# Kernel tuning notes

Measured on AMD Instinct MI355X. Metric: run time of the kernel, lower is better.

Reference implementation:

```python
import jax, jax.numpy as jnp
import numpy as np

N = 100000      # nodes
E = 1600000     # directed edges
F_IN = 128      # num_node_features
C = 10          # num_classes
EPS = 1e-5      # BatchNorm eps


def setup_inputs() -> dict:
    key = jax.random.key(0)
    ks = jax.random.split(key, 16)
    x = jax.random.normal(ks[0], (N, F_IN), jnp.float32)
    edge_index = jax.random.randint(ks[1], (2, E), 0, N, dtype=jnp.int32)

    def glorot(k, fi, fo):
        s = jnp.sqrt(6.0 / (fi + fo)).astype(jnp.float32)
        return jax.random.uniform(k, (fi, fo), jnp.float32, -s, s)

    return {
        "x": x, "edge_index": edge_index,
        "W1": glorot(ks[2], F_IN, 16), "b1": jnp.zeros((16,), jnp.float32),
        "g1": jnp.ones((16,), jnp.float32), "be1": jnp.zeros((16,), jnp.float32),
        "W2": glorot(ks[3], 16, 32), "b2": jnp.zeros((32,), jnp.float32),
        "g2": jnp.ones((32,), jnp.float32), "be2": jnp.zeros((32,), jnp.float32),
        "W3": glorot(ks[4], 32, 64), "b3": jnp.zeros((64,), jnp.float32),
        "g3": jnp.ones((64,), jnp.float32), "be3": jnp.zeros((64,), jnp.float32),
        "W4": glorot(ks[5], 64, C), "b4": jnp.zeros((C,), jnp.float32),
    }


def _gcn_conv(h, W, b, src, dst, norm):
    # GCNConv: transform then normalized scatter-add aggregation (with self-loops baked into src/dst/norm)
    h = h @ W                                   # [N, F_out]
    msg = h[src] * norm[:, None]                # [E+N, F_out] edge-gathered messages
    agg = jax.ops.segment_sum(msg, dst, num_segments=N)
    return agg + b


def _bn_gelu(h, g, be):
    # BatchNorm1d (training-mode batch stats, biased var) + exact GELU
    mu = h.mean(axis=0)
    var = ((h - mu) ** 2).mean(axis=0)
    return jax.nn.gelu((h - mu) * jax.lax.rsqrt(var + EPS) * g + be, approximate=False)


def reference(x, edge_index, W1, b1, g1, be1, W2, b2, g2, be2, W3, b3, g3, be3, W4, b4):
    src, dst = edge_index[0], edge_index[1]
    loop = jnp.arange(N, dtype=src.dtype)
    src = jnp.concatenate([src, loop])          # add self-loops
    dst = jnp.concatenate([dst, loop])
    deg = jax.ops.segment_sum(jnp.ones_like(dst, jnp.float32), dst, num_segments=N)
    dinv = jax.lax.rsqrt(deg)                   # deg >= 1 thanks to self-loops
    norm = dinv[src] * dinv[dst]                # D^-1/2 (A+I) D^-1/2 edge weights

    h = _bn_gelu(_gcn_conv(x, W1, b1, src, dst, norm), g1, be1)
    h = _bn_gelu(_gcn_conv(h, W2, b2, src, dst, norm), g2, be2)
    h = _bn_gelu(_gcn_conv(h, W3, b3, src, dst, norm), g3, be3)
    # dropout is identity in eval mode
    h = _gcn_conv(h, W4, b4, src, dst, norm)
    return jax.nn.log_softmax(h, axis=1)
```

## Files before the change

kernel.cpp:

```cpp
#include <hip/hip_runtime.h>
#include <math.h>


#define TPB 256
#define K_BUCK 256
#define CCHUNK 4096
#define DCAP 8192
constexpr float BN_EPS = 1e-5f;

#define SCHUNK 2048

__global__ void scan_reduce_kernel(const int* __restrict__ in, int* __restrict__ bsum, int n) {
    int base = blockIdx.x * SCHUNK;
    int s = 0;
    for (int j = threadIdx.x; j < SCHUNK; j += TPB) {
        int i = base + j;
        s += (i < n) ? in[i] : 0;
    }
#pragma unroll
    for (int d = 32; d; d >>= 1) s += __shfl_down(s, d);
    __shared__ int ws[TPB / 64];
    if ((threadIdx.x & 63) == 0) ws[threadIdx.x >> 6] = s;
    __syncthreads();
    if (threadIdx.x == 0) {
        int t = 0;
        for (int w = 0; w < TPB / 64; ++w) t += ws[w];
        bsum[blockIdx.x] = t;
    }
}

__global__ void scan_bsum_kernel(int* __restrict__ bsum, int nb) {
    __shared__ int carry;
    int lane = threadIdx.x;
    if (lane == 0) carry = 0;
    __syncthreads();
    for (int base = 0; base < nb; base += 64) {
        int i = base + lane;
        int v = (i < nb) ? bsum[i] : 0;
        int incl = v;
#pragma unroll
        for (int d = 1; d < 64; d <<= 1) {
            int u = __shfl_up(incl, d);
            if (lane >= d) incl += u;
        }
        if (i < nb) bsum[i] = carry + incl - v;
        int tot = __shfl(incl, 63);
        __syncthreads();
        if (lane == 0) carry += tot;
        __syncthreads();
    }
}

__global__ void scan_apply_kernel(const int* __restrict__ in, const int* __restrict__ bsum,
                                  int* __restrict__ out, int n) {
    int base = blockIdx.x * SCHUNK;
    int tid = threadIdx.x;
    int lane = tid & 63, wave = tid >> 6;
    int i0 = base + tid * 8;
    int v[8];
    int tsum = 0;
#pragma unroll
    for (int k = 0; k < 8; ++k) {
        int i = i0 + k;
        v[k] = (i < n) ? in[i] : 0;
        tsum += v[k];
    }
    int incl = tsum;
#pragma unroll
    for (int d = 1; d < 64; d <<= 1) {
        int u = __shfl_up(incl, d);
        if (lane >= d) incl += u;
    }
    int lexcl = incl - tsum;
    __shared__ int wsum[TPB / 64];
    if (lane == 63) wsum[wave] = incl;
    __syncthreads();
    int wbase = 0;
    for (int w = 0; w < wave; ++w) wbase += wsum[w];
    int off = bsum[blockIdx.x] + wbase + lexcl;
#pragma unroll
    for (int k = 0; k < 8; ++k) {
        int i = i0 + k;
        if (i < n) out[i] = off;
        off += v[k];
    }
}


__global__ void bucket_hist_kernel(const int* __restrict__ dst, int* __restrict__ hist,
                                   float* __restrict__ stats, int e, int n, int nb) {
    __shared__ int lh[K_BUCK];
    for (int i = threadIdx.x; i < K_BUCK; i += TPB) lh[i] = 0;
    if (blockIdx.x == 0)
        for (int i = threadIdx.x; i < 384; i += TPB) stats[i] = 0.0f;
    __syncthreads();
    int base = blockIdx.x * CCHUNK;
    int end = min(base + CCHUNK, e);
    int div = (n + K_BUCK - 1) / K_BUCK;
    for (int i = base + threadIdx.x; i < end; i += TPB) atomicAdd(&lh[dst[i] / div], 1);
    __syncthreads();
    for (int b = threadIdx.x; b < K_BUCK; b += TPB) hist[b * nb + blockIdx.x] = lh[b];
}

__global__ void bucket_scatter_kernel(const int* __restrict__ src, const int* __restrict__ dst,
                                      const int* __restrict__ hist, const int* __restrict__ hbase,
                                      int2* __restrict__ ebuf, int e, int n, int nb) {
    __shared__ int lbase[K_BUCK];
    __shared__ int eoff[K_BUCK];
    __shared__ int lcur[K_BUCK];
    __shared__ int2 stage[CCHUNK];
    int t = threadIdx.x;
    int blk = blockIdx.x;
    int c = hist[t * nb + blk];
    lbase[t] = hbase[t * nb + blk];
    lcur[t] = 0;
    eoff[t] = c;
    __syncthreads();
    for (int d = 1; d < K_BUCK; d <<= 1) {
        int v = (t >= d) ? eoff[t - d] : 0;
        __syncthreads();
        eoff[t] += v;
        __syncthreads();
    }
    eoff[t] -= c;
    __syncthreads();
    int base = blk * CCHUNK;
    int end = min(base + CCHUNK, e);
    int div = (n + K_BUCK - 1) / K_BUCK;
    for (int i = base + t; i < end; i += TPB) {
        int d = dst[i];
        int b = d / div;
        int p = atomicAdd(&lcur[b], 1);
        stage[eoff[b] + p] = make_int2(src[i], d);
    }
    __syncthreads();
    int cnt_here = end - base;
    for (int j = t; j < cnt_here; j += TPB) {
        int2 e2 = stage[j];
        int b = e2.y / div;
        ebuf[lbase[b] + (j - eoff[b])] = e2;
    }
}

__global__ void bucket_offsets_kernel(const int2* __restrict__ ebuf, const int* __restrict__ hbase,
                                      int* __restrict__ offsets, float* __restrict__ dinv,
                                      int e, int n, int nb) {
    __shared__ int lcnt[512];
    __shared__ int lexc[512];
    int b = blockIdx.x;
    int div = (n + K_BUCK - 1) / K_BUCK;
    int lo = b * div;
    int hi = min(lo + div, n);
    int nloc = hi - lo;
    int ebeg = hbase[b * nb];
    int eend = (b == K_BUCK - 1) ? e : hbase[(b + 1) * nb];
    for (int i = threadIdx.x; i < 512; i += TPB) lcnt[i] = 0;
    __syncthreads();
    for (int j = ebeg + threadIdx.x; j < eend; j += TPB)
        atomicAdd(&lcnt[ebuf[j].y - lo], 1);
    __syncthreads();
    if (threadIdx.x < 64) {
        int l = threadIdx.x;
        int base = l * 8;
        int v[8];
        int tsum = 0;
#pragma unroll
        for (int k = 0; k < 8; ++k) { v[k] = lcnt[base + k]; tsum += v[k]; }
        int incl = tsum;
#pragma unroll
        for (int d = 1; d < 64; d <<= 1) {
            int u = __shfl_up(incl, d);
            if (l >= d) incl += u;
        }
        int off = incl - tsum;
#pragma unroll
        for (int k = 0; k < 8; ++k) { lexc[base + k] = off; off += v[k]; }
    }
    __syncthreads();
    for (int i = threadIdx.x; i < nloc; i += TPB) {
        offsets[lo + i] = ebeg + lexc[i];
        dinv[lo + i] = rsqrtf((float)(lcnt[i] + 1));
    }
    if (b == K_BUCK - 1 && threadIdx.x == 0) offsets[n] = e;
}

__global__ void csr_fill_kernel(const int2* __restrict__ ebuf, const int* __restrict__ hbase,
                                const int* __restrict__ offsets, int* __restrict__ csr_src,
                                int e, int n, int nb) {
    __shared__ int lcur[400];
    __shared__ int lcsr[DCAP];
    int b = blockIdx.x;
    int div = (n + K_BUCK - 1) / K_BUCK;
    int lo = b * div;
    int hi = min(lo + div, n);
    int ebeg = hbase[b * nb];
    int eend = (b == K_BUCK - 1) ? e : hbase[(b + 1) * nb];
    int segbase = offsets[lo];
    int seglen = eend - ebeg;
    for (int i = threadIdx.x; i < hi - lo; i += TPB) lcur[i] = offsets[lo + i] - segbase;
    __syncthreads();
    for (int j = ebeg + threadIdx.x; j < eend; j += TPB) {
        int2 e2 = ebuf[j];
        int p = atomicAdd(&lcur[e2.y - lo], 1);
        if (p < DCAP) lcsr[p] = e2.x;
        else csr_src[segbase + p] = e2.x;
    }
    __syncthreads();
    int lim = min(seglen, DCAP);
    for (int j = threadIdx.x; j < lim; j += TPB) csr_src[segbase + j] = lcsr[j];
}


template <int FIN, int FOUT, bool DINV>
__global__ void gemm_rw_kernel(const float* __restrict__ H, const float* __restrict__ W,
                               float* __restrict__ O, const float* __restrict__ dinv, int n) {
    int row = blockIdx.x * blockDim.x + threadIdx.x;
    if (row >= n) return;
    float acc[FOUT];
#pragma unroll
    for (int c = 0; c < FOUT; ++c) acc[c] = 0.0f;
    const float4* h4 = (const float4*)(H + (size_t)row * FIN);
#pragma unroll
    for (int k = 0; k < FIN / 4; ++k) {
        float4 h = h4[k];
        const float* w = W + (size_t)(4 * k) * FOUT;
#pragma unroll
        for (int c = 0; c < FOUT; ++c) {
            acc[c] = fmaf(h.x, w[c], acc[c]);
            acc[c] = fmaf(h.y, w[FOUT + c], acc[c]);
            acc[c] = fmaf(h.z, w[2 * FOUT + c], acc[c]);
            acc[c] = fmaf(h.w, w[3 * FOUT + c], acc[c]);
        }
    }
    float sc = DINV ? dinv[row] : 1.0f;
    float4* o4 = (float4*)(O + (size_t)row * FOUT);
#pragma unroll
    for (int c = 0; c < FOUT / 4; ++c)
        o4[c] = make_float4(acc[4 * c] * sc, acc[4 * c + 1] * sc,
                            acc[4 * c + 2] * sc, acc[4 * c + 3] * sc);
}

__global__ void gemm_l4_kernel(const float* __restrict__ H, const float* __restrict__ W,
                               float* __restrict__ O, const float* __restrict__ dinv, int n) {
    int row = blockIdx.x * blockDim.x + threadIdx.x;
    if (row >= n) return;
    float acc[10];
#pragma unroll
    for (int c = 0; c < 10; ++c) acc[c] = 0.0f;
    const float4* h4 = (const float4*)(H + (size_t)row * 64);
#pragma unroll
    for (int k = 0; k < 16; ++k) {
        float4 h = h4[k];
        const float* w = W + (size_t)(4 * k) * 10;
#pragma unroll
        for (int c = 0; c < 10; ++c) {
            acc[c] = fmaf(h.x, w[c], acc[c]);
            acc[c] = fmaf(h.y, w[10 + c], acc[c]);
            acc[c] = fmaf(h.z, w[20 + c], acc[c]);
            acc[c] = fmaf(h.w, w[30 + c], acc[c]);
        }
    }
    float sc = dinv[row];
    float4* o4 = (float4*)(O + (size_t)row * 16);
    o4[0] = make_float4(acc[0] * sc, acc[1] * sc, acc[2] * sc, acc[3] * sc);
    o4[1] = make_float4(acc[4] * sc, acc[5] * sc, acc[6] * sc, acc[7] * sc);
    o4[2] = make_float4(acc[8] * sc, acc[9] * sc, 0.0f, 0.0f);
}

template <int F>
__global__ void bn_stats_kernel(const float* __restrict__ V, float* __restrict__ stats, int n) {
    constexpr int RPB = TPB / F;
    int f = threadIdx.x % F;
    int rl = threadIdx.x / F;
    float s = 0.0f, s2 = 0.0f;
    for (int r = blockIdx.x * RPB + rl; r < n; r += gridDim.x * RPB) {
        float v = V[(size_t)r * F + f];
        s += v;
        s2 = fmaf(v, v, s2);
    }
    __shared__ float sh[2 * F];
    for (int i = threadIdx.x; i < 2 * F; i += TPB) sh[i] = 0.0f;
    __syncthreads();
    atomicAdd(&sh[f], s);
    atomicAdd(&sh[F + f], s2);
    __syncthreads();
    for (int i = threadIdx.x; i < 2 * F; i += TPB) atomicAdd(&stats[i], sh[i]);
}


template <int F, bool STATS>
__global__ void agg4_kernel(const float* __restrict__ T, float* __restrict__ A,
                            const float* __restrict__ dinv, const int* __restrict__ offsets,
                            const int* __restrict__ csr_src, float* __restrict__ stats, int n) {
    constexpr int G = F / 4;
    __shared__ float sh[STATS ? 2 * F : 1];
    if (STATS) {
        for (int i = threadIdx.x; i < 2 * F; i += blockDim.x) sh[i] = 0.0f;
        __syncthreads();
    }
    const float4* T4 = (const float4*)T;
    float4 ss = {0, 0, 0, 0}, s2 = {0, 0, 0, 0};
    int lane0 = -1;
    int total = n * G;
    int stride = gridDim.x * blockDim.x;
    for (int idx = blockIdx.x * blockDim.x + threadIdx.x; idx < total; idx += stride) {
        int node = idx / G;
        int lane = idx % G;
        float4 acc = T4[(size_t)node * G + lane];
        int s = offsets[node], e = offsets[node + 1];
        int j = s;
        for (; j + 3 < e; j += 4) {
            int u0 = csr_src[j], u1 = csr_src[j + 1], u2 = csr_src[j + 2], u3 = csr_src[j + 3];
            float4 t0 = T4[(size_t)u0 * G + lane];
            float4 t1 = T4[(size_t)u1 * G + lane];
            float4 t2 = T4[(size_t)u2 * G + lane];
            float4 t3 = T4[(size_t)u3 * G + lane];
            acc.x += (t0.x + t1.x) + (t2.x + t3.x);
            acc.y += (t0.y + t1.y) + (t2.y + t3.y);
            acc.z += (t0.z + t1.z) + (t2.z + t3.z);
            acc.w += (t0.w + t1.w) + (t2.w + t3.w);
        }
        for (; j < e; ++j) {
            int u = csr_src[j];
            float4 t = T4[(size_t)u * G + lane];
            acc.x += t.x; acc.y += t.y; acc.z += t.z; acc.w += t.w;
        }
        float di = dinv[node];
        acc.x *= di; acc.y *= di; acc.z *= di; acc.w *= di;
        ((float4*)A)[(size_t)idx] = acc;
        if (STATS) {
            ss.x += acc.x; ss.y += acc.y; ss.z += acc.z; ss.w += acc.w;
            s2.x = fmaf(acc.x, acc.x, s2.x); s2.y = fmaf(acc.y, acc.y, s2.y);
            s2.z = fmaf(acc.z, acc.z, s2.z); s2.w = fmaf(acc.w, acc.w, s2.w);
            lane0 = lane;
        }
    }
    if (STATS) {
        if (lane0 >= 0) {
            atomicAdd(&sh[lane0 * 4 + 0], ss.x); atomicAdd(&sh[lane0 * 4 + 1], ss.y);
            atomicAdd(&sh[lane0 * 4 + 2], ss.z); atomicAdd(&sh[lane0 * 4 + 3], ss.w);
            atomicAdd(&sh[F + lane0 * 4 + 0], s2.x); atomicAdd(&sh[F + lane0 * 4 + 1], s2.y);
            atomicAdd(&sh[F + lane0 * 4 + 2], s2.z); atomicAdd(&sh[F + lane0 * 4 + 3], s2.w);
        }
        __syncthreads();
        for (int i = threadIdx.x; i < 2 * F; i += blockDim.x) atomicAdd(&stats[i], sh[i]);
    }
}

__global__ void agg_lsm_kernel(const float* __restrict__ T, const float* __restrict__ dinv,
                               const int* __restrict__ offsets, const int* __restrict__ csr_src,
                               const float* __restrict__ b4, float* __restrict__ out, int n) {
    int idx = blockIdx.x * blockDim.x + threadIdx.x;
    int node = idx >> 2;
    int lane = idx & 3;
    if (node >= n) return;
    const float4* T4 = (const float4*)T;
    float4 acc = T4[(size_t)node * 4 + lane];
    int s = offsets[node], e = offsets[node + 1];
    int j = s;
    for (; j + 1 < e; j += 2) {
        int u0 = csr_src[j], u1 = csr_src[j + 1];
        float4 t0 = T4[(size_t)u0 * 4 + lane];
        float4 t1 = T4[(size_t)u1 * 4 + lane];
        acc.x += t0.x + t1.x; acc.y += t0.y + t1.y;
        acc.z += t0.z + t1.z; acc.w += t0.w + t1.w;
    }
    if (j < e) {
        int u = csr_src[j];
        float4 t = T4[(size_t)u * 4 + lane];
        acc.x += t.x; acc.y += t.y; acc.z += t.z; acc.w += t.w;
    }
    float di = dinv[node];
    int c0 = lane * 4;
    float v[4];
    int nv = (c0 < 10) ? min(10 - c0, 4) : 0;
#pragma unroll
    for (int k = 0; k < 4; ++k) {
        float a = (k == 0) ? acc.x : (k == 1) ? acc.y : (k == 2) ? acc.z : acc.w;
        v[k] = (k < nv) ? fmaf(di, a, b4[c0 + k]) : -1e30f;
    }
    float m = fmaxf(fmaxf(v[0], v[1]), fmaxf(v[2], v[3]));
    m = fmaxf(m, __shfl_xor(m, 1));
    m = fmaxf(m, __shfl_xor(m, 2));
    float sum = 0.0f;
#pragma unroll
    for (int k = 0; k < 4; ++k)
        if (k < nv) sum += expf(v[k] - m);
    sum += __shfl_xor(sum, 1);
    sum += __shfl_xor(sum, 2);
    float ls = m + logf(sum);
#pragma unroll
    for (int k = 0; k < 4; ++k)
        if (k < nv) out[(size_t)node * 10 + c0 + k] = v[k] - ls;
}


template <int F, bool DINV>
__global__ void bn_gelu_kernel(float* __restrict__ V, const float* __restrict__ stats,
                               const float* __restrict__ g, const float* __restrict__ be,
                               const float* __restrict__ dinv, int n) {
    int i = blockIdx.x * blockDim.x + threadIdx.x;
    if (i >= n * F) return;
    int f = i % F;
    float inv_n = 1.0f / (float)n;
    float mu = stats[f] * inv_n;
    float var = stats[F + f] * inv_n - mu * mu;
    float sc = rsqrtf(var + BN_EPS) * g[f];
    float shf = be[f] - mu * sc;
    float x = fmaf(V[i], sc, shf);
    float y = 0.5f * x * (1.0f + erff(x * 0.70710678118654752f));
    V[i] = DINV ? y * dinv[i / F] : y;
}

static inline int cdiv(long long a, int b) { return (int)((a + b - 1) / b); }

extern "C" void kernel_launch(void* const* d_in, const int* in_sizes, int n_in,
                              void* d_out, int out_size, void* d_ws, size_t ws_size,
                              hipStream_t stream) {
    const float* x  = (const float*)d_in[0];
    const int*   ei = (const int*)d_in[1];
    const float* W1 = (const float*)d_in[2];
    const float* g1 = (const float*)d_in[4];
    const float* be1= (const float*)d_in[5];
    const float* W2 = (const float*)d_in[6];
    const float* g2 = (const float*)d_in[8];
    const float* be2= (const float*)d_in[9];
    const float* W3 = (const float*)d_in[10];
    const float* g3 = (const float*)d_in[12];
    const float* be3= (const float*)d_in[13];
    const float* W4 = (const float*)d_in[14];
    const float* b4 = (const float*)d_in[15];
    float* out = (float*)d_out;

    const int N = in_sizes[0] / 128;
    const int E = in_sizes[1] / 2;
    const int* srcI = ei;
    const int* dstI = ei + E;
    const int NBc = cdiv(E, CCHUNK);
    const int HN  = K_BUCK * NBc;
    const int NBh = cdiv(HN, SCHUNK);

    char* p = (char*)d_ws;
    auto carve = [&](size_t bytes) {
        void* q = (void*)p;
        p += (bytes + 255) & ~(size_t)255;
        return q;
    };
    int*   offsets = (int*)  carve((size_t)(N + 1) * 4);
    float* dinv    = (float*)carve((size_t)N * 4);
    int*   csr_src = (int*)  carve((size_t)E * 4);
    int*   hist    = (int*)  carve((size_t)HN * 4);
    int*   hbase   = (int*)  carve((size_t)(HN + 1) * 4);
    int2*  ebuf    = (int2*) carve((size_t)E * 8);
    int*   bsum    = (int*)  carve((size_t)(NBh + 1) * 4);
    float* stats   = (float*)carve(384 * 4);
    float* A       = (float*)carve((size_t)N * 64 * 4);
    float* B       = (float*)carve((size_t)N * 64 * 4);

    bucket_hist_kernel<<<NBc, TPB, 0, stream>>>(dstI, hist, stats, E, N, NBc);
    scan_reduce_kernel<<<NBh, TPB, 0, stream>>>(hist, bsum, HN);
    scan_bsum_kernel<<<1, 64, 0, stream>>>(bsum, NBh);
    scan_apply_kernel<<<NBh, TPB, 0, stream>>>(hist, bsum, hbase, HN);
    bucket_scatter_kernel<<<NBc, TPB, 0, stream>>>(srcI, dstI, hist, hbase, ebuf, E, N, NBc);
    bucket_offsets_kernel<<<K_BUCK, TPB, 0, stream>>>(ebuf, hbase, offsets, dinv, E, N, NBc);
    csr_fill_kernel<<<K_BUCK, TPB, 0, stream>>>(ebuf, hbase, offsets, csr_src, E, N, NBc);

    gemm_rw_kernel<128, 16, true><<<cdiv(N, TPB), TPB, 0, stream>>>(x, W1, A, dinv, N);
    agg4_kernel<16, true><<<1024, TPB, 0, stream>>>(A, B, dinv, offsets, csr_src, stats + 0, N);
    bn_gelu_kernel<16, true><<<cdiv((long long)N * 16, TPB), TPB, 0, stream>>>(B, stats + 0, g1, be1, dinv, N);

    agg4_kernel<16, false><<<cdiv((long long)N * 4, TPB), TPB, 0, stream>>>(B, A, dinv, offsets, csr_src, nullptr, N);
    gemm_rw_kernel<16, 32, false><<<cdiv(N, TPB), TPB, 0, stream>>>(A, W2, B, nullptr, N);
    bn_stats_kernel<32><<<256, TPB, 0, stream>>>(B, stats + 128, N);
    bn_gelu_kernel<32, true><<<cdiv((long long)N * 32, TPB), TPB, 0, stream>>>(B, stats + 128, g2, be2, dinv, N);

    agg4_kernel<32, false><<<cdiv((long long)N * 8, TPB), TPB, 0, stream>>>(B, A, dinv, offsets, csr_src, nullptr, N);
    gemm_rw_kernel<32, 64, false><<<cdiv(N, TPB), TPB, 0, stream>>>(A, W3, B, nullptr, N);
    bn_stats_kernel<64><<<256, TPB, 0, stream>>>(B, stats + 256, N);
    bn_gelu_kernel<64, false><<<cdiv((long long)N * 64, TPB), TPB, 0, stream>>>(B, stats + 256, g3, be3, nullptr, N);

    gemm_l4_kernel<<<cdiv(N, TPB), TPB, 0, stream>>>(B, W4, A, dinv, N);
    agg_lsm_kernel<<<cdiv((long long)N * 4, TPB), TPB, 0, stream>>>(A, dinv, offsets, csr_src, b4, out, N);
}
```

Before: 411.2 us.

## Pack edges into 32-bit words, merge CSR build kernels, fuse BN-GELU into final GEMM

Edges in the bucket buffer are packed into one 32-bit word holding the local destination offset and the source index, which halves the buffer traffic. The offsets and CSR fill kernels become a single kernel, so the buffer is read once less and one launch goes away. The layer-3 BatchNorm and GELU are applied inside the final 64x10 GEMM, which removes a full read and write of the N x 64 activation. The cost is per-row recomputation of the BN scale and an erf for each element in the GEMM, and the packing assumes source indices fit in 23 bits and local destinations fit in 9 bits.

```diff
diff --git a/kernel.cpp b/kernel.cpp
--- a/kernel.cpp
+++ b/kernel.cpp
@@ -6,6 +6,8 @@
 #define K_BUCK 256
 #define CCHUNK 4096
 #define DCAP 8192
+#define SRC_BITS 23
+#define SRC_MASK 0x7FFFFF
 constexpr float BN_EPS = 1e-5f;
 
 #define SCHUNK 2048
@@ -104,11 +106,12 @@
 
 __global__ void bucket_scatter_kernel(const int* __restrict__ src, const int* __restrict__ dst,
                                       const int* __restrict__ hist, const int* __restrict__ hbase,
-                                      int2* __restrict__ ebuf, int e, int n, int nb) {
+                                      unsigned int* __restrict__ ebuf, int e, int n, int nb) {
     __shared__ int lbase[K_BUCK];
     __shared__ int eoff[K_BUCK];
     __shared__ int lcur[K_BUCK];
-    __shared__ int2 stage[CCHUNK];
+    __shared__ unsigned int stage[CCHUNK];
+    __shared__ unsigned char sb[CCHUNK];
     int t = threadIdx.x;
     int blk = blockIdx.x;
     int c = hist[t * nb + blk];
@@ -130,23 +133,27 @@
     for (int i = base + t; i < end; i += TPB) {
         int d = dst[i];
         int b = d / div;
+        unsigned int w = ((unsigned int)(d - b * div) << SRC_BITS) | (unsigned int)src[i];
         int p = atomicAdd(&lcur[b], 1);
-        stage[eoff[b] + p] = make_int2(src[i], d);
+        int sp = eoff[b] + p;
+        stage[sp] = w;
+        sb[sp] = (unsigned char)b;
     }
     __syncthreads();
     int cnt_here = end - base;
     for (int j = t; j < cnt_here; j += TPB) {
-        int2 e2 = stage[j];
-        int b = e2.y / div;
-        ebuf[lbase[b] + (j - eoff[b])] = e2;
-    }
-}
-
-__global__ void bucket_offsets_kernel(const int2* __restrict__ ebuf, const int* __restrict__ hbase,
-                                      int* __restrict__ offsets, float* __restrict__ dinv,
-                                      int e, int n, int nb) {
+        int b = sb[j];
+        ebuf[lbase[b] + (j - eoff[b])] = stage[j];
+    }
+}
+
+__global__ void bucket_build_kernel(const unsigned int* __restrict__ ebuf,
+                                    const int* __restrict__ hbase, int* __restrict__ offsets,
+                                    float* __restrict__ dinv, int* __restrict__ csr_src,
+                                    int e, int n, int nb) {
     __shared__ int lcnt[512];
-    __shared__ int lexc[512];
+    __shared__ int lcur[512];
+    __shared__ int lcsr[DCAP];
     int b = blockIdx.x;
     int div = (n + K_BUCK - 1) / K_BUCK;
     int lo = b * div;
@@ -157,7 +164,7 @@
     for (int i = threadIdx.x; i < 512; i += TPB) lcnt[i] = 0;
     __syncthreads();
     for (int j = ebeg + threadIdx.x; j < eend; j += TPB)
-        atomicAdd(&lcnt[ebuf[j].y - lo], 1);
+        atomicAdd(&lcnt[ebuf[j] >> SRC_BITS], 1);
     __syncthreads();
     if (threadIdx.x < 64) {
         int l = threadIdx.x;
@@ -174,40 +181,25 @@
         }
         int off = incl - tsum;
 #pragma unroll
-        for (int k = 0; k < 8; ++k) { lexc[base + k] = off; off += v[k]; }
+        for (int k = 0; k < 8; ++k) { lcur[base + k] = off; off += v[k]; }
     }
     __syncthreads();
     for (int i = threadIdx.x; i < nloc; i += TPB) {
-        offsets[lo + i] = ebeg + lexc[i];
+        offsets[lo + i] = ebeg + lcur[i];
         dinv[lo + i] = rsqrtf((float)(lcnt[i] + 1));
     }
     if (b == K_BUCK - 1 && threadIdx.x == 0) offsets[n] = e;
-}
-
-__global__ void csr_fill_kernel(const int2* __restrict__ ebuf, const int* __restrict__ hbase,
-                                const int* __restrict__ offsets, int* __restrict__ csr_src,
-                                int e, int n, int nb) {
-    __shared__ int lcur[400];
-    __shared__ int lcsr[DCAP];
-    int b = blockIdx.x;
-    int div = (n + K_BUCK - 1) / K_BUCK;
-    int lo = b * div;
-    int hi = min(lo + div, n);
-    int ebeg = hbase[b * nb];
-    int eend = (b == K_BUCK - 1) ? e : hbase[(b + 1) * nb];
-    int segbase = offsets[lo];
+    __syncthreads();
+    for (int j = ebeg + threadIdx.x; j < eend; j += TPB) {
+        unsigned int w = ebuf[j];
+        int p = atomicAdd(&lcur[w >> SRC_BITS], 1);
+        if (p < DCAP) lcsr[p] = (int)(w & SRC_MASK);
+        else csr_src[ebeg + p] = (int)(w & SRC_MASK);
+    }
+    __syncthreads();
     int seglen = eend - ebeg;
-    for (int i = threadIdx.x; i < hi - lo; i += TPB) lcur[i] = offsets[lo + i] - segbase;
-    __syncthreads();
-    for (int j = ebeg + threadIdx.x; j < eend; j += TPB) {
-        int2 e2 = ebuf[j];
-        int p = atomicAdd(&lcur[e2.y - lo], 1);
-        if (p < DCAP) lcsr[p] = e2.x;
-        else csr_src[segbase + p] = e2.x;
-    }
-    __syncthreads();
     int lim = min(seglen, DCAP);
-    for (int j = threadIdx.x; j < lim; j += TPB) csr_src[segbase + j] = lcsr[j];
+    for (int j = threadIdx.x; j < lim; j += TPB) csr_src[ebeg + j] = lcsr[j];
 }
 
 
@@ -240,10 +232,13 @@
                             acc[4 * c + 2] * sc, acc[4 * c + 3] * sc);
 }
 
-__global__ void gemm_l4_kernel(const float* __restrict__ H, const float* __restrict__ W,
-                               float* __restrict__ O, const float* __restrict__ dinv, int n) {
+__global__ void gemm_l4_fused_kernel(const float* __restrict__ H, const float* __restrict__ W,
+                                     float* __restrict__ O, const float* __restrict__ dinv,
+                                     const float* __restrict__ stats, const float* __restrict__ g,
+                                     const float* __restrict__ be, int n) {
     int row = blockIdx.x * blockDim.x + threadIdx.x;
     if (row >= n) return;
+    float inv_n = 1.0f / (float)n;
     float acc[10];
 #pragma unroll
     for (int c = 0; c < 10; ++c) acc[c] = 0.0f;
@@ -251,13 +246,24 @@
 #pragma unroll
     for (int k = 0; k < 16; ++k) {
         float4 h = h4[k];
+        float hv[4] = {h.x, h.y, h.z, h.w};
+#pragma unroll
+        for (int j = 0; j < 4; ++j) {
+            int f = 4 * k + j;
+            float mu = stats[f] * inv_n;
+            float var = stats[64 + f] * inv_n - mu * mu;
+            float scf = rsqrtf(var + BN_EPS) * g[f];
+            float shf = be[f] - mu * scf;
+            float x = fmaf(hv[j], scf, shf);
+            hv[j] = 0.5f * x * (1.0f + erff(x * 0.70710678118654752f));
+        }
         const float* w = W + (size_t)(4 * k) * 10;
 #pragma unroll
         for (int c = 0; c < 10; ++c) {
-            acc[c] = fmaf(h.x, w[c], acc[c]);
-            acc[c] = fmaf(h.y, w[10 + c], acc[c]);
-            acc[c] = fmaf(h.z, w[20 + c], acc[c]);
-            acc[c] = fmaf(h.w, w[30 + c], acc[c]);
+            acc[c] = fmaf(hv[0], w[c], acc[c]);
+            acc[c] = fmaf(hv[1], w[10 + c], acc[c]);
+            acc[c] = fmaf(hv[2], w[20 + c], acc[c]);
+            acc[c] = fmaf(hv[3], w[30 + c], acc[c]);
         }
     }
     float sc = dinv[row];
@@ -451,7 +457,7 @@
     int*   csr_src = (int*)  carve((size_t)E * 4);
     int*   hist    = (int*)  carve((size_t)HN * 4);
     int*   hbase   = (int*)  carve((size_t)(HN + 1) * 4);
-    int2*  ebuf    = (int2*) carve((size_t)E * 8);
+    unsigned int* ebuf = (unsigned int*)carve((size_t)E * 4);
     int*   bsum    = (int*)  carve((size_t)(NBh + 1) * 4);
     float* stats   = (float*)carve(384 * 4);
     float* A       = (float*)carve((size_t)N * 64 * 4);
@@ -462,8 +468,7 @@
     scan_bsum_kernel<<<1, 64, 0, stream>>>(bsum, NBh);
     scan_apply_kernel<<<NBh, TPB, 0, stream>>>(hist, bsum, hbase, HN);
     bucket_scatter_kernel<<<NBc, TPB, 0, stream>>>(srcI, dstI, hist, hbase, ebuf, E, N, NBc);
-    bucket_offsets_kernel<<<K_BUCK, TPB, 0, stream>>>(ebuf, hbase, offsets, dinv, E, N, NBc);
-    csr_fill_kernel<<<K_BUCK, TPB, 0, stream>>>(ebuf, hbase, offsets, csr_src, E, N, NBc);
+    bucket_build_kernel<<<K_BUCK, TPB, 0, stream>>>(ebuf, hbase, offsets, dinv, csr_src, E, N, NBc);
 
     gemm_rw_kernel<128, 16, true><<<cdiv(N, TPB), TPB, 0, stream>>>(x, W1, A, dinv, N);
     agg4_kernel<16, true><<<1024, TPB, 0, stream>>>(A, B, dinv, offsets, csr_src, stats + 0, N);
@@ -477,8 +482,7 @@
     agg4_kernel<32, false><<<cdiv((long long)N * 8, TPB), TPB, 0, stream>>>(B, A, dinv, offsets, csr_src, nullptr, N);
     gemm_rw_kernel<32, 64, false><<<cdiv(N, TPB), TPB, 0, stream>>>(A, W3, B, nullptr, N);
     bn_stats_kernel<64><<<256, TPB, 0, stream>>>(B, stats + 256, N);
-    bn_gelu_kernel<64, false><<<cdiv((long long)N * 64, TPB), TPB, 0, stream>>>(B, stats + 256, g3, be3, nullptr, N);
-
-    gemm_l4_kernel<<<cdiv(N, TPB), TPB, 0, stream>>>(B, W4, A, dinv, N);
+
+    gemm_l4_fused_kernel<<<cdiv(N, TPB), TPB, 0, stream>>>(B, W4, A, dinv, stats + 256, g3, be3, N);
     agg_lsm_kernel<<<cdiv((long long)N * 4, TPB), TPB, 0, stream>>>(A, dinv, offsets, csr_src, b4, out, N);
 }
```

Result: slower. 450.2 us (+9.5%).
